# Kernel optimization log

Measured on AMD Instinct MI355X. Metric: run time of the kernel, lower is better.

The kernel has to match this reference:

```python
import jax, jax.numpy as jnp
import numpy as np

B, NPER, F, D, E, NUM_STEPS = 256, 512, 256, 32, 524288, 4
N = B * NPER
INIT_TAU, TAU_SCALE, STEP_ALPHA = 0.1, 0.5, 5.0


def setup_inputs() -> dict:
    key = jax.random.key(0)
    ks = jax.random.split(key, 10)
    x_start = jax.random.uniform(ks[0], (N,), jnp.float32, 0.1, 1.0)   # strictly positive iterate
    x_solution = jax.random.uniform(ks[1], (N,), jnp.float32, 0.0, 1.0)
    q = jax.random.normal(ks[2], (N,), jnp.float32)
    edge_src = jax.random.randint(ks[3], (E,), 0, N, jnp.int32)
    edge_dst = jax.random.randint(ks[4], (E,), 0, N, jnp.int32)
    vals_batch = jnp.repeat(jnp.arange(B, dtype=jnp.int32), NPER)      # equal-sized graphs
    proj_matrix = jax.random.normal(ks[5], (B, NPER, F), jnp.float32) / np.float32(np.sqrt(NPER))
    W_in = jax.random.normal(ks[6], (2, D), jnp.float32) / np.float32(np.sqrt(2.0))
    b_in = jnp.zeros((D,), jnp.float32)
    W_msg = jax.random.normal(ks[7], (D, D), jnp.float32) / np.float32(np.sqrt(D))
    b_msg = jnp.zeros((D,), jnp.float32)
    W_out = jax.random.normal(ks[8], (D, 1), jnp.float32) / np.float32(np.sqrt(D))
    b_out = jnp.zeros((1,), jnp.float32)
    return {"x_start": x_start, "x_solution": x_solution, "q": q,
            "proj_matrix": proj_matrix, "W_in": W_in, "b_in": b_in,
            "W_msg": W_msg, "b_msg": b_msg, "W_out": W_out, "b_out": b_out,
            "edge_src": edge_src, "edge_dst": edge_dst, "vals_batch": vals_batch}


def _l1_normalize(x, batch):
    # per-graph L1 normalization: x / sum_i |x_i| over the graph segment
    s = jax.ops.segment_sum(jnp.abs(x), batch, num_segments=B)
    return x / (s[batch] + 1e-12)


def _line_search(x, d, batch, max_alpha):
    # largest per-graph alpha s.t. x + alpha*d >= 0, capped at max_alpha
    ratio = jnp.where(d < 0, x / jnp.maximum(-d, 1e-12), max_alpha)
    a = jnp.clip(jax.ops.segment_min(ratio, batch, num_segments=B), 0.0, max_alpha)
    return a[batch]  # gathered back to per-node


def _gnn(xs, q, edge_src, edge_dst, W_in, b_in, W_msg, b_msg, W_out, b_out):
    h = jax.nn.relu(jnp.stack([xs, q], axis=-1) @ W_in + b_in)      # [N, D]
    m = h[edge_src] @ W_msg + b_msg                                  # [E, D]
    agg = jax.ops.segment_sum(m, edge_dst, num_segments=N)          # [N, D]
    h2 = jax.nn.relu(h + agg)
    return h2 @ W_out[:, 0] + b_out[0]                               # [N]


def reference(x_start, x_solution, q, proj_matrix, W_in, b_in, W_msg, b_msg,
              W_out, b_out, edge_src, edge_dst, vals_batch):
    tau = INIT_TAU
    xs = x_start
    preds, labels = [], []
    for _ in range(NUM_STEPS):
        pred = _gnn(xs, q, edge_src, edge_dst, W_in, b_in, W_msg, b_msg, W_out, b_out)
        preds.append(pred)
        labels.append(_l1_normalize(x_solution - xs, vals_batch))
        p = _l1_normalize(jax.lax.stop_gradient(pred), vals_batch)   # .detach() in torch
        direction = p + 3.0 * tau / (xs + tau)
        tau = max(tau * TAU_SCALE, 1e-5)
        # to_dense_batch with equal graph sizes == reshape; project onto nullspace basis
        dd = direction.reshape(B, NPER)
        df = jnp.einsum('bnf,bn->bf', proj_matrix, dd)               # [B, F]
        pproj = jnp.einsum('bnf,bf->bn', proj_matrix, df).reshape(-1)  # [N]
        alpha = _line_search(xs, pproj, vals_batch, STEP_ALPHA) * 0.995
        xs = xs + alpha * pproj
    return jnp.stack(preds, axis=1), jnp.stack(labels, axis=1)       # each [N, NUM_STEPS]
```

## Files before the change

### kernel.cpp

```cpp
#include <hip/hip_runtime.h>

#define BB 256
#define NPER 512
#define FF 256
#define DD 32
#define EE 524288
#define NN (BB*NPER)
#define NSTEPS 4

__device__ __forceinline__ float bflo(unsigned u) { return __uint_as_float(u << 16); }
__device__ __forceinline__ float bfhi(unsigned u) { return __uint_as_float(u & 0xFFFF0000u); }


__global__ void k_deg(const int* __restrict__ dst, unsigned* __restrict__ deg) {
    int e = blockIdx.x * blockDim.x + threadIdx.x;
    atomicAdd(&deg[dst[e]], 1u);
}

__global__ void k_bsum(const unsigned* __restrict__ deg, unsigned* __restrict__ bsum) {
    __shared__ unsigned r[256];
    int t = threadIdx.x;
    r[t] = deg[blockIdx.x * 256 + t];
    __syncthreads();
    for (int o = 128; o > 0; o >>= 1) { if (t < o) r[t] += r[t + o]; __syncthreads(); }
    if (t == 0) bsum[blockIdx.x] = r[0];
}

__global__ void k_scanb(const unsigned* __restrict__ bsum, unsigned* __restrict__ bbase) {
    __shared__ unsigned r[512];
    int t = threadIdx.x;
    unsigned own = bsum[t];
    r[t] = own;
    __syncthreads();
    for (int o = 1; o < 512; o <<= 1) {
        unsigned v = (t >= o) ? r[t - o] : 0u;
        __syncthreads();
        r[t] += v;
        __syncthreads();
    }
    bbase[t] = r[t] - own;
}

__global__ void k_offsets(const unsigned* __restrict__ deg, const unsigned* __restrict__ bbase,
                          unsigned* __restrict__ rowstart, unsigned* __restrict__ cursor) {
    __shared__ unsigned r[256];
    int t = threadIdx.x;
    int i = blockIdx.x * 256 + t;
    unsigned d = deg[i];
    r[t] = d;
    __syncthreads();
    for (int o = 1; o < 256; o <<= 1) {
        unsigned v = (t >= o) ? r[t - o] : 0u;
        __syncthreads();
        r[t] += v;
        __syncthreads();
    }
    unsigned excl = r[t] - d + bbase[blockIdx.x];
    rowstart[i] = excl;
    cursor[i] = excl;
}

__global__ void k_fill(const int* __restrict__ src, const int* __restrict__ dst,
                       unsigned* __restrict__ cursor, int* __restrict__ csr_src) {
    int e = blockIdx.x * blockDim.x + threadIdx.x;
    unsigned pos = atomicAdd(&cursor[dst[e]], 1u);
    csr_src[pos] = src[e];
}

__global__ void k_cast(const float* __restrict__ P, unsigned* __restrict__ Pbf2) {
    size_t i = (size_t)(blockIdx.x * blockDim.x + threadIdx.x);
    float4 p = ((const float4*)P)[i];
    unsigned u0 = __float_as_uint(p.x), u1 = __float_as_uint(p.y);
    unsigned u2 = __float_as_uint(p.z), u3 = __float_as_uint(p.w);
    u0 = (u0 + 0x7FFFu + ((u0 >> 16) & 1u)) >> 16;
    u1 = (u1 + 0x7FFFu + ((u1 >> 16) & 1u)) >> 16;
    u2 = (u2 + 0x7FFFu + ((u2 >> 16) & 1u)) >> 16;
    u3 = (u3 + 0x7FFFu + ((u3 >> 16) & 1u)) >> 16;
    uint2 o; o.x = u0 | (u1 << 16); o.y = u2 | (u3 << 16);
    ((uint2*)Pbf2)[i] = o;
}

__global__ void k_pack(const float* __restrict__ xs0, const float* __restrict__ q,
                       float2* __restrict__ xq) {
    int i = blockIdx.x * blockDim.x + threadIdx.x;
    float2 v; v.x = xs0[i]; v.y = q[i];
    xq[i] = v;
}


__global__ void k_node_g(const float2* __restrict__ xq,
                         const float* __restrict__ Win, const float* __restrict__ bin,
                         const unsigned* __restrict__ rowstart, const unsigned* __restrict__ deg,
                         const int* __restrict__ csr_src,
                         const float* __restrict__ Wmsg, const float* __restrict__ bmsg,
                         const float* __restrict__ Wout, const float* __restrict__ bout,
                         float* __restrict__ pred, float* __restrict__ out_preds, int step) {
    int tid = threadIdx.x;
    int d = tid & 31;
    int i = blockIdx.x * 8 + (tid >> 5);
    float w0 = Win[d], w1 = Win[DD + d], b0 = bin[d];
    float wcol[DD];
    #pragma unroll
    for (int k = 0; k < DD; ++k) wcol[k] = Wmsg[k * DD + d];
    unsigned rs = rowstart[i];
    unsigned dg = deg[i];
    unsigned nfull = dg < 32u ? dg : 32u;
    float xv = 0.f, qv = 0.f;
    if ((unsigned)d < nfull) {
        int sv = csr_src[rs + d];
        float2 v = xq[sv];
        xv = v.x; qv = v.y;
    }
    float s = 0.f;
    for (unsigned j = 0; j < nfull; ++j) {
        float xj = __shfl(xv, (int)j, 32);
        float qj = __shfl(qv, (int)j, 32);
        s += fmaxf(xj * w0 + qj * w1 + b0, 0.f);
    }
    for (unsigned j = 32; j < dg; ++j) {
        int sv = csr_src[rs + j];
        float2 v = xq[sv];
        s += fmaxf(v.x * w0 + v.y * w1 + b0, 0.f);
    }
    float2 self = xq[i];
    float hval = fmaxf(self.x * w0 + self.y * w1 + b0, 0.f);
    float agg = (float)dg * bmsg[d];
    #pragma unroll
    for (int k = 0; k < DD; ++k) agg += __shfl(s, k, 32) * wcol[k];
    float h2 = fmaxf(hval + agg, 0.f);
    float v = h2 * Wout[d];
    for (int o = 16; o > 0; o >>= 1) v += __shfl_down(v, o, 32);
    if (d == 0) {
        float pr = v + bout[0];
        pred[i] = pr;
        out_preds[i * NSTEPS + step] = pr;
    }
}

__global__ void k_graph(const float2* __restrict__ xq, const float* __restrict__ xsol,
                        const float* __restrict__ pred,
                        float* __restrict__ out_labels, float* __restrict__ dd,
                        float* __restrict__ df,
                        unsigned int* __restrict__ alphaMin, float tau, int step) {
    __shared__ float s1[8], s2[8];
    int b = blockIdx.x;
    int t = threadIdx.x;
    int wid = t >> 6;
    int lane = t & 63;
    int i = b * NPER + t;
    float x = xq[i].x;
    float r = xsol[i] - x;
    float p = pred[i];
    float a1 = fabsf(r), a2 = fabsf(p);
    #pragma unroll
    for (int o = 32; o > 0; o >>= 1) {
        a1 += __shfl_down(a1, o, 64);
        a2 += __shfl_down(a2, o, 64);
    }
    if (lane == 0) { s1[wid] = a1; s2[wid] = a2; }
    __syncthreads();
    float Sr = 1e-12f, Sp = 1e-12f;
    #pragma unroll
    for (int k = 0; k < 8; ++k) { Sr += s1[k]; Sp += s2[k]; }
    out_labels[i * NSTEPS + step] = r / Sr;
    dd[i] = p / Sp + 3.0f * tau / (x + tau);
    if (t < FF) df[b * FF + t] = 0.f;
    if (t == 0) alphaMin[b] = 0x7f800000u;
}

__global__ void k_df(const unsigned short* __restrict__ Pbf, const float* __restrict__ dd,
                     float* __restrict__ df) {
    __shared__ float dl[128];
    __shared__ float sl[4 * FF];
    int b = blockIdx.x >> 2, sp = blockIdx.x & 3;
    int t = threadIdx.x, w = t >> 6, lane = t & 63;
    if (t < 128) dl[t] = dd[b * NPER + sp * 128 + t];
    __syncthreads();
    const uint2* P2 = (const uint2*)(Pbf + (size_t)(b * NPER + sp * 128 + w * 32) * FF) + lane;
    float4 acc = {0.f, 0.f, 0.f, 0.f};
    const float* dw = &dl[w * 32];
    #pragma unroll 4
    for (int n = 0; n < 32; ++n) {
        uint2 pv = P2[(size_t)n * 64];
        float sc = dw[n];
        acc.x += bflo(pv.x) * sc; acc.y += bfhi(pv.x) * sc;
        acc.z += bflo(pv.y) * sc; acc.w += bfhi(pv.y) * sc;
    }
    ((float4*)sl)[w * 64 + lane] = acc;
    __syncthreads();
    float v = sl[t] + sl[FF + t] + sl[2 * FF + t] + sl[3 * FF + t];
    atomicAdd(&df[b * FF + t], v);
}

__global__ void k_pproj(const unsigned short* __restrict__ Pbf, const float* __restrict__ df,
                        const float2* __restrict__ xq,
                        float* __restrict__ pproj, unsigned int* __restrict__ alphaMin) {
    __shared__ float mred[4];
    int t = threadIdx.x, w = t >> 6, lane = t & 63;
    int hl = lane >> 5, l5 = lane & 31;
    int b = blockIdx.x >> 4;
    const float4* dfp4 = (const float4*)(df + (size_t)b * FF);
    float4 dfa = dfp4[l5 * 2], dfb = dfp4[l5 * 2 + 1];
    int n0 = blockIdx.x * 32 + w * 8 + hl;
    float m = 5.0f;
    #pragma unroll
    for (int it = 0; it < 4; ++it) {
        int n = n0 + it * 2;
        uint4 pv = ((const uint4*)(Pbf + (size_t)n * FF))[l5];
        float acc = bflo(pv.x) * dfa.x + bfhi(pv.x) * dfa.y
                  + bflo(pv.y) * dfa.z + bfhi(pv.y) * dfa.w
                  + bflo(pv.z) * dfb.x + bfhi(pv.z) * dfb.y
                  + bflo(pv.w) * dfb.z + bfhi(pv.w) * dfb.w;
        #pragma unroll
        for (int o = 16; o > 0; o >>= 1) acc += __shfl_down(acc, o, 32);
        if (l5 == 0) {
            pproj[n] = acc;
            float x = xq[n].x;
            float ratio = (acc < 0.f) ? (x / fmaxf(-acc, 1e-12f)) : 5.0f;
            m = fminf(m, ratio);
        }
    }
    m = fminf(m, __shfl_xor(m, 32, 64));
    if (lane == 0) mred[w] = m;
    __syncthreads();
    if (t == 0) {
        float mm = fminf(fminf(mred[0], mred[1]), fminf(mred[2], mred[3]));
        atomicMin(&alphaMin[b], __float_as_uint(mm));
    }
}

__global__ void k_update(const unsigned int* __restrict__ alphaMin,
                         const float* __restrict__ pproj, float2* __restrict__ xq) {
    int i = blockIdx.x * blockDim.x + threadIdx.x;
    int b = i >> 9;
    float a = __uint_as_float(alphaMin[b]);
    a = fminf(fmaxf(a, 0.f), 5.0f) * 0.995f;
    xq[i].x += a * pproj[i];
}


extern "C" void kernel_launch(void* const* d_in, const int* in_sizes, int n_in,
                              void* d_out, int out_size, void* d_ws, size_t ws_size,
                              hipStream_t stream) {
    const float* x_start = (const float*)d_in[0];
    const float* x_sol   = (const float*)d_in[1];
    const float* q       = (const float*)d_in[2];
    const float* P       = (const float*)d_in[3];
    const float* Win     = (const float*)d_in[4];
    const float* bin     = (const float*)d_in[5];
    const float* Wmsg    = (const float*)d_in[6];
    const float* bmsg    = (const float*)d_in[7];
    const float* Wout    = (const float*)d_in[8];
    const float* bout    = (const float*)d_in[9];
    const int*   esrc    = (const int*)d_in[10];
    const int*   edst    = (const int*)d_in[11];

    float* out_preds  = (float*)d_out;
    float* out_labels = (float*)d_out + (size_t)NN * NSTEPS;

    float* w = (float*)d_ws;
    float2* xq  = (float2*)w; w += 2 * (size_t)NN;
    float* pred  = w; w += NN;
    float* ddv   = w; w += NN;
    float* pproj = w; w += NN;
    float* df    = w; w += (size_t)BB * FF;
    unsigned* alphaMin = (unsigned*)w; w += BB;
    unsigned* deg      = (unsigned*)w; w += NN;
    unsigned* rowstart = (unsigned*)w; w += NN;
    unsigned* cursor   = (unsigned*)w; w += NN;
    unsigned* bsum     = (unsigned*)w; w += NN / 256;
    unsigned* bbase    = (unsigned*)w; w += NN / 256;
    int* csr_src       = (int*)w;      w += EE;
    unsigned short* Pbf = (unsigned short*)w;

    hipMemsetAsync(deg, 0, NN * sizeof(unsigned), stream);
    k_deg<<<EE / 256, 256, 0, stream>>>(edst, deg);
    k_cast<<<(BB * NPER * FF / 4) / 256, 256, 0, stream>>>(P, (unsigned*)Pbf);
    k_pack<<<NN / 256, 256, 0, stream>>>(x_start, q, xq);
    k_bsum<<<NN / 256, 256, 0, stream>>>(deg, bsum);
    k_scanb<<<1, NN / 256, 0, stream>>>(bsum, bbase);
    k_offsets<<<NN / 256, 256, 0, stream>>>(deg, bbase, rowstart, cursor);
    k_fill<<<EE / 256, 256, 0, stream>>>(esrc, edst, cursor, csr_src);

    float tau = 0.1f;
    for (int step = 0; step < NSTEPS; ++step) {
        k_node_g<<<NN / 8, 256, 0, stream>>>(xq, Win, bin, rowstart, deg, csr_src,
                                             Wmsg, bmsg, Wout, bout, pred, out_preds, step);
        k_graph<<<BB, NPER, 0, stream>>>(xq, x_sol, pred, out_labels, ddv, df, alphaMin,
                                         tau, step);
        if (step < NSTEPS - 1) {
            k_df<<<BB * 4, 256, 0, stream>>>(Pbf, ddv, df);
            k_pproj<<<NN / 32, 256, 0, stream>>>(Pbf, df, xq, pproj, alphaMin);
            k_update<<<NN / 256, 256, 0, stream>>>(alphaMin, pproj, xq);
        }
        tau = fmaxf(tau * 0.5f, 1e-5f);
    }
}
```

Measured before the change: 525.3 us.

## Fuse per-graph normalize, projection, line search and update into one block kernel

Replaces k_graph, k_df, k_pproj and k_update with one kernel that runs one 512-thread block per graph. The block keeps direction, df, pproj and the alpha reduction in shared memory, which removes the global atomics and intermediate buffers. The bf16 cast of the projection matrix moves into step 0 of this kernel, fused with the first df pass, and the x/q pack is merged into the degree kernel. The trade-off is only 256 blocks, which may leave the GPU underoccupied while each block streams 256KB of P twice, and step 0 still uses exact fp32 P for df.

```diff
diff --git a/kernel.cpp b/kernel.cpp
--- a/kernel.cpp
+++ b/kernel.cpp
@@ -10,11 +10,17 @@
 
 __device__ __forceinline__ float bflo(unsigned u) { return __uint_as_float(u << 16); }
 __device__ __forceinline__ float bfhi(unsigned u) { return __uint_as_float(u & 0xFFFF0000u); }
-
-
-__global__ void k_deg(const int* __restrict__ dst, unsigned* __restrict__ deg) {
-    int e = blockIdx.x * blockDim.x + threadIdx.x;
-    atomicAdd(&deg[dst[e]], 1u);
+__device__ __forceinline__ unsigned rtn_bf16(unsigned u) {
+    return (u + 0x7FFFu + ((u >> 16) & 1u)) >> 16;
+}
+
+
+__global__ void k_degpack(const int* __restrict__ dst, unsigned* __restrict__ deg,
+                          const float* __restrict__ xs0, const float* __restrict__ q,
+                          float2* __restrict__ xq) {
+    int t = blockIdx.x * blockDim.x + threadIdx.x;
+    if (t < NN) { float2 v; v.x = xs0[t]; v.y = q[t]; xq[t] = v; }
+    atomicAdd(&deg[dst[t]], 1u);
 }
 
 __global__ void k_bsum(const unsigned* __restrict__ deg, unsigned* __restrict__ bsum) {
@@ -65,26 +71,6 @@
     int e = blockIdx.x * blockDim.x + threadIdx.x;
     unsigned pos = atomicAdd(&cursor[dst[e]], 1u);
     csr_src[pos] = src[e];
-}
-
-__global__ void k_cast(const float* __restrict__ P, unsigned* __restrict__ Pbf2) {
-    size_t i = (size_t)(blockIdx.x * blockDim.x + threadIdx.x);
-    float4 p = ((const float4*)P)[i];
-    unsigned u0 = __float_as_uint(p.x), u1 = __float_as_uint(p.y);
-    unsigned u2 = __float_as_uint(p.z), u3 = __float_as_uint(p.w);
-    u0 = (u0 + 0x7FFFu + ((u0 >> 16) & 1u)) >> 16;
-    u1 = (u1 + 0x7FFFu + ((u1 >> 16) & 1u)) >> 16;
-    u2 = (u2 + 0x7FFFu + ((u2 >> 16) & 1u)) >> 16;
-    u3 = (u3 + 0x7FFFu + ((u3 >> 16) & 1u)) >> 16;
-    uint2 o; o.x = u0 | (u1 << 16); o.y = u2 | (u3 << 16);
-    ((uint2*)Pbf2)[i] = o;
-}
-
-__global__ void k_pack(const float* __restrict__ xs0, const float* __restrict__ q,
-                       float2* __restrict__ xq) {
-    int i = blockIdx.x * blockDim.x + threadIdx.x;
-    float2 v; v.x = xs0[i]; v.y = q[i];
-    xq[i] = v;
 }
 
 
@@ -137,16 +123,21 @@
     }
 }
 
-__global__ void k_graph(const float2* __restrict__ xq, const float* __restrict__ xsol,
-                        const float* __restrict__ pred,
-                        float* __restrict__ out_labels, float* __restrict__ dd,
-                        float* __restrict__ df,
-                        unsigned int* __restrict__ alphaMin, float tau, int step) {
-    __shared__ float s1[8], s2[8];
+__global__ __launch_bounds__(512) void k_step(const float* __restrict__ Pf,
+                                              unsigned short* __restrict__ Pbf,
+                                              float2* __restrict__ xq,
+                                              const float* __restrict__ xsol,
+                                              const float* __restrict__ pred,
+                                              float* __restrict__ out_labels,
+                                              float tau, int step) {
+    __shared__ float ddl[NPER];
+    __shared__ float sl[8 * FF];
+    __shared__ float dfl[FF];
+    __shared__ float pp[NPER];
+    __shared__ float red[8], red2[8];
     int b = blockIdx.x;
     int t = threadIdx.x;
-    int wid = t >> 6;
-    int lane = t & 63;
+    int w = t >> 6, lane = t & 63;
     int i = b * NPER + t;
     float x = xq[i].x;
     float r = xsol[i] - x;
@@ -157,85 +148,83 @@
         a1 += __shfl_down(a1, o, 64);
         a2 += __shfl_down(a2, o, 64);
     }
-    if (lane == 0) { s1[wid] = a1; s2[wid] = a2; }
+    if (lane == 0) { red[w] = a1; red2[w] = a2; }
     __syncthreads();
     float Sr = 1e-12f, Sp = 1e-12f;
     #pragma unroll
-    for (int k = 0; k < 8; ++k) { Sr += s1[k]; Sp += s2[k]; }
+    for (int k = 0; k < 8; ++k) { Sr += red[k]; Sp += red2[k]; }
     out_labels[i * NSTEPS + step] = r / Sr;
-    dd[i] = p / Sp + 3.0f * tau / (x + tau);
-    if (t < FF) df[b * FF + t] = 0.f;
-    if (t == 0) alphaMin[b] = 0x7f800000u;
-}
-
-__global__ void k_df(const unsigned short* __restrict__ Pbf, const float* __restrict__ dd,
-                     float* __restrict__ df) {
-    __shared__ float dl[128];
-    __shared__ float sl[4 * FF];
-    int b = blockIdx.x >> 2, sp = blockIdx.x & 3;
-    int t = threadIdx.x, w = t >> 6, lane = t & 63;
-    if (t < 128) dl[t] = dd[b * NPER + sp * 128 + t];
-    __syncthreads();
-    const uint2* P2 = (const uint2*)(Pbf + (size_t)(b * NPER + sp * 128 + w * 32) * FF) + lane;
+    if (step == NSTEPS - 1) return;
+    ddl[t] = p / Sp + 3.0f * tau / (x + tau);
+    __syncthreads();
+
     float4 acc = {0.f, 0.f, 0.f, 0.f};
-    const float* dw = &dl[w * 32];
+    size_t rowbase = (size_t)(b * NPER + w * 64) * FF;
+    if (step == 0) {
+        const float4* Pr = (const float4*)(Pf + rowbase) + lane;
+        uint2* Pw = (uint2*)(Pbf + rowbase) + lane;
+        #pragma unroll 4
+        for (int n = 0; n < 64; ++n) {
+            float4 pv = Pr[(size_t)n * 64];
+            float sc = ddl[w * 64 + n];
+            acc.x += pv.x * sc; acc.y += pv.y * sc;
+            acc.z += pv.z * sc; acc.w += pv.w * sc;
+            unsigned u0 = rtn_bf16(__float_as_uint(pv.x));
+            unsigned u1 = rtn_bf16(__float_as_uint(pv.y));
+            unsigned u2 = rtn_bf16(__float_as_uint(pv.z));
+            unsigned u3 = rtn_bf16(__float_as_uint(pv.w));
+            uint2 o; o.x = u0 | (u1 << 16); o.y = u2 | (u3 << 16);
+            Pw[(size_t)n * 64] = o;
+        }
+    } else {
+        const uint2* Pr = (const uint2*)(Pbf + rowbase) + lane;
+        #pragma unroll 8
+        for (int n = 0; n < 64; ++n) {
+            uint2 pv = Pr[(size_t)n * 64];
+            float sc = ddl[w * 64 + n];
+            acc.x += bflo(pv.x) * sc; acc.y += bfhi(pv.x) * sc;
+            acc.z += bflo(pv.y) * sc; acc.w += bfhi(pv.y) * sc;
+        }
+    }
+    ((float4*)sl)[w * 64 + lane] = acc;
+    __syncthreads();
+    if (t < FF) {
+        float v = 0.f;
+        #pragma unroll
+        for (int k = 0; k < 8; ++k) v += sl[k * FF + t];
+        dfl[t] = v;
+    }
+    __syncthreads();
+
+    int g = t >> 5, l5 = t & 31;
+    float4 dfa = ((const float4*)dfl)[l5 * 2];
+    float4 dfb = ((const float4*)dfl)[l5 * 2 + 1];
+    const uint4* Pr4 = (const uint4*)(Pbf + (size_t)(b * NPER + g * 32) * FF) + l5;
     #pragma unroll 4
-    for (int n = 0; n < 32; ++n) {
-        uint2 pv = P2[(size_t)n * 64];
-        float sc = dw[n];
-        acc.x += bflo(pv.x) * sc; acc.y += bfhi(pv.x) * sc;
-        acc.z += bflo(pv.y) * sc; acc.w += bfhi(pv.y) * sc;
-    }
-    ((float4*)sl)[w * 64 + lane] = acc;
-    __syncthreads();
-    float v = sl[t] + sl[FF + t] + sl[2 * FF + t] + sl[3 * FF + t];
-    atomicAdd(&df[b * FF + t], v);
-}
-
-__global__ void k_pproj(const unsigned short* __restrict__ Pbf, const float* __restrict__ df,
-                        const float2* __restrict__ xq,
-                        float* __restrict__ pproj, unsigned int* __restrict__ alphaMin) {
-    __shared__ float mred[4];
-    int t = threadIdx.x, w = t >> 6, lane = t & 63;
-    int hl = lane >> 5, l5 = lane & 31;
-    int b = blockIdx.x >> 4;
-    const float4* dfp4 = (const float4*)(df + (size_t)b * FF);
-    float4 dfa = dfp4[l5 * 2], dfb = dfp4[l5 * 2 + 1];
-    int n0 = blockIdx.x * 32 + w * 8 + hl;
-    float m = 5.0f;
-    #pragma unroll
-    for (int it = 0; it < 4; ++it) {
-        int n = n0 + it * 2;
-        uint4 pv = ((const uint4*)(Pbf + (size_t)n * FF))[l5];
-        float acc = bflo(pv.x) * dfa.x + bfhi(pv.x) * dfa.y
-                  + bflo(pv.y) * dfa.z + bfhi(pv.y) * dfa.w
-                  + bflo(pv.z) * dfb.x + bfhi(pv.z) * dfb.y
-                  + bflo(pv.w) * dfb.z + bfhi(pv.w) * dfb.w;
+    for (int it = 0; it < 32; ++it) {
+        uint4 pv = Pr4[(size_t)it * 32];
+        float a = bflo(pv.x) * dfa.x + bfhi(pv.x) * dfa.y
+                + bflo(pv.y) * dfa.z + bfhi(pv.y) * dfa.w
+                + bflo(pv.z) * dfb.x + bfhi(pv.z) * dfb.y
+                + bflo(pv.w) * dfb.z + bfhi(pv.w) * dfb.w;
         #pragma unroll
-        for (int o = 16; o > 0; o >>= 1) acc += __shfl_down(acc, o, 32);
-        if (l5 == 0) {
-            pproj[n] = acc;
-            float x = xq[n].x;
-            float ratio = (acc < 0.f) ? (x / fmaxf(-acc, 1e-12f)) : 5.0f;
-            m = fminf(m, ratio);
-        }
-    }
-    m = fminf(m, __shfl_xor(m, 32, 64));
-    if (lane == 0) mred[w] = m;
-    __syncthreads();
-    if (t == 0) {
-        float mm = fminf(fminf(mred[0], mred[1]), fminf(mred[2], mred[3]));
-        atomicMin(&alphaMin[b], __float_as_uint(mm));
-    }
-}
-
-__global__ void k_update(const unsigned int* __restrict__ alphaMin,
-                         const float* __restrict__ pproj, float2* __restrict__ xq) {
-    int i = blockIdx.x * blockDim.x + threadIdx.x;
-    int b = i >> 9;
-    float a = __uint_as_float(alphaMin[b]);
-    a = fminf(fmaxf(a, 0.f), 5.0f) * 0.995f;
-    xq[i].x += a * pproj[i];
+        for (int o = 16; o > 0; o >>= 1) a += __shfl_down(a, o, 32);
+        if (l5 == 0) pp[g * 32 + it] = a;
+    }
+    __syncthreads();
+
+    float d = pp[t];
+    float ratio = (d < 0.f) ? (x / fmaxf(-d, 1e-12f)) : 5.0f;
+    float m = ratio;
+    #pragma unroll
+    for (int o = 32; o > 0; o >>= 1) m = fminf(m, __shfl_down(m, o, 64));
+    if (lane == 0) red[w] = m;
+    __syncthreads();
+    float mm = red[0];
+    #pragma unroll
+    for (int k = 1; k < 8; ++k) mm = fminf(mm, red[k]);
+    float alpha = fminf(fmaxf(mm, 0.f), 5.0f) * 0.995f;
+    xq[i].x = x + alpha * d;
 }
 
 
@@ -261,10 +250,6 @@
     float* w = (float*)d_ws;
     float2* xq  = (float2*)w; w += 2 * (size_t)NN;
     float* pred  = w; w += NN;
-    float* ddv   = w; w += NN;
-    float* pproj = w; w += NN;
-    float* df    = w; w += (size_t)BB * FF;
-    unsigned* alphaMin = (unsigned*)w; w += BB;
     unsigned* deg      = (unsigned*)w; w += NN;
     unsigned* rowstart = (unsigned*)w; w += NN;
     unsigned* cursor   = (unsigned*)w; w += NN;
@@ -274,9 +259,7 @@
     unsigned short* Pbf = (unsigned short*)w;
 
     hipMemsetAsync(deg, 0, NN * sizeof(unsigned), stream);
-    k_deg<<<EE / 256, 256, 0, stream>>>(edst, deg);
-    k_cast<<<(BB * NPER * FF / 4) / 256, 256, 0, stream>>>(P, (unsigned*)Pbf);
-    k_pack<<<NN / 256, 256, 0, stream>>>(x_start, q, xq);
+    k_degpack<<<EE / 256, 256, 0, stream>>>(edst, deg, x_start, q, xq);
     k_bsum<<<NN / 256, 256, 0, stream>>>(deg, bsum);
     k_scanb<<<1, NN / 256, 0, stream>>>(bsum, bbase);
     k_offsets<<<NN / 256, 256, 0, stream>>>(deg, bbase, rowstart, cursor);
@@ -286,13 +269,7 @@
     for (int step = 0; step < NSTEPS; ++step) {
         k_node_g<<<NN / 8, 256, 0, stream>>>(xq, Win, bin, rowstart, deg, csr_src,
                                              Wmsg, bmsg, Wout, bout, pred, out_preds, step);
-        k_graph<<<BB, NPER, 0, stream>>>(xq, x_sol, pred, out_labels, ddv, df, alphaMin,
-                                         tau, step);
-        if (step < NSTEPS - 1) {
-            k_df<<<BB * 4, 256, 0, stream>>>(Pbf, ddv, df);
-            k_pproj<<<NN / 32, 256, 0, stream>>>(Pbf, df, xq, pproj, alphaMin);
-            k_update<<<NN / 256, 256, 0, stream>>>(alphaMin, pproj, xq);
-        }
+        k_step<<<BB, 512, 0, stream>>>(P, Pbf, xq, x_sol, pred, out_labels, tau, step);
         tau = fmaxf(tau * 0.5f, 1e-5f);
     }
 }
```

New measurement: 514.2 us. 1.02x faster.
